# Performance work log

Hardware: AMD Instinct MI355X
Metric: run time of the kernel (lower is better)

Reference implementation:

```python
import jax, jax.numpy as jnp
import numpy as np

SCALE = 1.0 / (100.0 ** 0.5)  # module hard-codes QK / sqrt(100)


def setup_inputs() -> dict:
    key = jax.random.key(0)
    k1, k2, k3 = jax.random.split(key, 3)
    B, S, D = 8, 2048, 512
    head_size = 64
    x = jax.random.normal(k1, (B, S, D), dtype=jnp.float32)
    kernel = jax.random.normal(k2, (3, D, head_size), dtype=jnp.float32) * 0.02
    dense = jax.random.normal(k3, (D, D), dtype=jnp.float32) * 0.02
    return {"x": x, "kernel": kernel, "dense": dense, "heads": 8}


def reference(x, kernel, dense, heads):
    # All heads use the SAME kernel slices in the original loop, so each
    # iteration produces an identical V; compute once and tile.
    WQ = jnp.einsum('bsd,dh->bsh', x, kernel[0])  # [B,S,Hd]
    WK = jnp.einsum('bsd,dh->bsh', x, kernel[1])
    WV = jnp.einsum('bsd,dh->bsh', x, kernel[2])
    scores = jnp.einsum('bqh,bkh->bqk', WQ, WK) * SCALE  # [B,S,S]
    attn = jax.nn.softmax(scores, axis=-1)
    V = jnp.einsum('bqk,bkh->bqh', attn, WV)  # [B,S,Hd]
    out = jnp.tile(V, (1, 1, heads))  # concat of identical heads -> [B,S,heads*Hd]
    return jnp.einsum('bsf,fo->bso', out, dense)
```

## Files before the change

kernel.cpp:

```cpp
#include <hip/hip_runtime.h>
#include <math.h>


typedef __bf16 bf16;
typedef __bf16 bf16x4v __attribute__((ext_vector_type(4)));
typedef __bf16 bf16x8v __attribute__((ext_vector_type(8)));
typedef float f32x4 __attribute__((ext_vector_type(4)));

namespace {
constexpr int kS = 2048;
constexpr int kD = 512;
constexpr int kH = 64;
constexpr int kRows = 16384;
}

#define MFMA16(a, b, c) __builtin_amdgcn_mfma_f32_16x16x32_bf16((a), (b), (c), 0, 0, 0)

__global__ __launch_bounds__(256) void prep_kernel(const float* __restrict__ w,
                                                   const float* __restrict__ dense,
                                                   bf16* __restrict__ wtg,
                                                   float* __restrict__ dr) {
  int idx = blockIdx.x * 256 + threadIdx.x;
  if (idx < 98304) {
    int mat = idx >> 15, rem = idx & 32767;
    int n = rem >> 9, k = rem & 511;
    wtg[idx] = (bf16)w[mat * 32768 + k * 64 + n];
  } else {
    int e = idx - 98304;
    int j = e >> 9, o = e & 511;
    float s = 0.f;
#pragma unroll
    for (int h = 0; h < 8; ++h) s += dense[(size_t)(h * 64 + j) * kD + o];
    dr[e] = s;
  }
}

__global__ __launch_bounds__(256) void proj_kernel(const float* __restrict__ x,
                                                   const bf16* __restrict__ wtg,
                                                   bf16* __restrict__ wq,
                                                   bf16* __restrict__ wk,
                                                   bf16* __restrict__ wvt) {
  const int bt = blockIdx.x;
  const int tid = threadIdx.x;
  const int w = tid >> 6, tx = tid & 15, quad = (tid >> 4) & 3;
  const int row0 = bt * 64;

  __shared__ bf16 Xs[64 * 72];
  __shared__ bf16 Wts[3 * 64 * 72];

  f32x4 acc[3][4];
#pragma unroll
  for (int m = 0; m < 3; ++m)
#pragma unroll
    for (int nt = 0; nt < 4; ++nt) acc[m][nt] = (f32x4){0.f, 0.f, 0.f, 0.f};

  for (int k0 = 0; k0 < kD; k0 += 64) {
    __syncthreads();
#pragma unroll
    for (int p = 0; p < 4; ++p) {
      int i4 = tid + p * 256;
      int r = i4 >> 4, c4 = (i4 & 15) * 4;
      float4 f = *(const float4*)&x[(size_t)(row0 + r) * kD + k0 + c4];
      bf16x4v h = {(bf16)f.x, (bf16)f.y, (bf16)f.z, (bf16)f.w};
      *(bf16x4v*)&Xs[r * 72 + c4] = h;
    }
#pragma unroll
    for (int p = 0; p < 6; ++p) {
      int cc = tid + p * 256;
      int mat = cc >> 9, rem = cc & 511;
      int n = rem >> 3, c8 = (rem & 7) * 8;
      *(uint4*)&Wts[(mat * 64 + n) * 72 + c8] =
          *(const uint4*)&wtg[(size_t)mat * 32768 + (size_t)n * 512 + k0 + c8];
    }
    __syncthreads();
#pragma unroll
    for (int s = 0; s < 2; ++s) {
      bf16x8v a = *(bf16x8v*)&Xs[(w * 16 + tx) * 72 + s * 32 + quad * 8];
#pragma unroll
      for (int m = 0; m < 3; ++m)
#pragma unroll
        for (int nt = 0; nt < 4; ++nt) {
          bf16x8v bfr =
              *(bf16x8v*)&Wts[(m * 64 + nt * 16 + tx) * 72 + s * 32 + quad * 8];
          acc[m][nt] = MFMA16(a, bfr, acc[m][nt]);
        }
    }
  }

#pragma unroll
  for (int nt = 0; nt < 4; ++nt)
#pragma unroll
    for (int r = 0; r < 4; ++r) {
      int row_g = row0 + w * 16 + quad * 4 + r;
      int col = nt * 16 + tx;
      wq[(size_t)row_g * 64 + col] = (bf16)acc[0][nt][r];
      wk[(size_t)row_g * 64 + col] = (bf16)acc[1][nt][r];
    }
  __syncthreads();
  bf16* Vt = Xs;
#pragma unroll
  for (int nt = 0; nt < 4; ++nt)
#pragma unroll
    for (int r = 0; r < 4; ++r)
      Vt[(nt * 16 + tx) * 72 + (w * 16 + quad * 4 + r)] = (bf16)acc[2][nt][r];
  __syncthreads();
#pragma unroll
  for (int p = 0; p < 2; ++p) {
    int c = tid + p * 256;
    int v = c >> 3, seg = c & 7;
    *(uint4*)&wvt[(size_t)v * kRows + row0 + seg * 8] =
        *(uint4*)&Vt[v * 72 + seg * 8];
  }
}

__global__ __launch_bounds__(256, 4) void flash_kernel(
    const bf16* __restrict__ wq, const bf16* __restrict__ wk,
    const bf16* __restrict__ wvt, float* __restrict__ vo) {
  const int bid = blockIdx.x;
  const int b = bid & 7, qb = bid >> 3;
  const int q0 = qb * 16;
  const int tid = threadIdx.x;
  const int w = tid >> 6, lane = tid & 63, tx = tid & 15, quad = (tid >> 4) & 3;

  __shared__ __align__(16) char lds[38912];
  bf16* Qs = (bf16*)lds;
  bf16* Ksw = (bf16*)(lds + 2048 + w * 4096);
  bf16* Vtw = (bf16*)(lds + 18432 + w * 4096);
  bf16* Psw = (bf16*)(lds + 34816 + w * 1024);

  const bf16* wqb = wq + (size_t)(b * kS) * 64;
  const bf16* wkb = wk + (size_t)(b * kS) * 64;
  const bf16* wvb = wvt + b * kS;

  if (tid < 128) {
    int r = tid >> 3, lc = tid & 7;
    *(uint4*)&Qs[r * 64 + ((lc ^ (r & 7)) * 8)] =
        *(const uint4*)&wqb[(size_t)(q0 + r) * 64 + lc * 8];
  }
  __syncthreads();

  const int kc0 = (quad ^ (tx & 7)) * 8;
  const int kc1 = ((4 + quad) ^ (tx & 7)) * 8;
  const int h2 = (tx ^ (tx >> 2)) & 3;

  bf16x8v aq0 = *(bf16x8v*)&Qs[tx * 64 + kc0];
  bf16x8v aq1 = *(bf16x8v*)&Qs[tx * 64 + kc1];

  f32x4 oacc[4];
#pragma unroll
  for (int nt = 0; nt < 4; ++nt) oacc[nt] = (f32x4){0.f, 0.f, 0.f, 0.f};
  float lsum[4] = {0.f, 0.f, 0.f, 0.f};

  const int ksr = lane >> 3, kslc = lane & 7;
  const int vsv = lane >> 2, vsck = lane & 3;

  for (int t = 0; t < 16; ++t) {
    const int k0 = (t * 4 + w) * 32;
#pragma unroll
    for (int j = 0; j < 4; ++j) {
      int r = ksr + j * 8;
      *(uint4*)&Ksw[r * 64 + ((kslc ^ (r & 7)) * 8)] =
          *(const uint4*)&wkb[(size_t)(k0 + r) * 64 + kslc * 8];
      int v = vsv + j * 16;
      *(uint4*)&Vtw[v * 32 + ((vsck ^ ((v ^ (v >> 2)) & 3)) * 8)] =
          *(const uint4*)&wvb[(size_t)v * kRows + k0 + vsck * 8];
    }

#pragma unroll
    for (int nt = 0; nt < 2; ++nt) {
      int krow = nt * 16 + tx;
      bf16x8v b0 = *(bf16x8v*)&Ksw[krow * 64 + kc0];
      bf16x8v b1 = *(bf16x8v*)&Ksw[krow * 64 + kc1];
      f32x4 z = (f32x4){0.f, 0.f, 0.f, 0.f};
      z = MFMA16(aq0, b0, z);
      z = MFMA16(aq1, b1, z);
#pragma unroll
      for (int r = 0; r < 4; ++r) {
        float p = __expf(z[r] * 0.1f);
        lsum[r] += p;
        int q = quad * 4 + r;
        int chunk = nt * 2 + (tx >> 3);
        Psw[q * 32 + ((chunk ^ (r ^ quad)) * 8) + (tx & 7)] = (bf16)p;
      }
    }

    bf16x8v pa = *(bf16x8v*)&Psw[tx * 32 + ((quad ^ h2) * 8)];
#pragma unroll
    for (int nt = 0; nt < 4; ++nt) {
      bf16x8v vb = *(bf16x8v*)&Vtw[(nt * 16 + tx) * 32 + ((quad ^ h2) * 8)];
      oacc[nt] = MFMA16(pa, vb, oacc[nt]);
    }
  }

  __syncthreads();
  float* myO = (float*)(lds + 2048 + w * 4096);
  float* myL = (float*)(lds + 18432 + w * 64);
#pragma unroll
  for (int nt = 0; nt < 4; ++nt)
#pragma unroll
    for (int r = 0; r < 4; ++r)
      myO[(quad * 4 + r) * 64 + nt * 16 + tx] = oacc[nt][r];
#pragma unroll
  for (int r = 0; r < 4; ++r) {
    float v = lsum[r];
#pragma unroll
    for (int m = 1; m < 16; m <<= 1) v += __shfl_xor(v, m, 64);
    if (tx == 0) myL[quad * 4 + r] = v;
  }
  __syncthreads();

#pragma unroll
  for (int p = 0; p < 4; ++p) {
    int e = tid + p * 256;
    int row = e >> 6;
    float s = 0.f, lt = 0.f;
#pragma unroll
    for (int wv = 0; wv < 4; ++wv) {
      s += ((const float*)(lds + 2048 + wv * 4096))[e];
      lt += ((const float*)(lds + 18432 + wv * 64))[row];
    }
    vo[(size_t)(b * kS + q0 + row) * 64 + (e & 63)] = s / lt;
  }
}

__global__ __launch_bounds__(256) void out_gemm_kernel(
    const float* __restrict__ v, const float* __restrict__ dr,
    float* __restrict__ out) {
  const int rt = blockIdx.x, ct = blockIdx.y;
  const int tid = threadIdx.x;
  const int tx = tid & 15, ty = tid >> 4;

  __shared__ float As[64][68];
  __shared__ float Bs[64][68];

#pragma unroll
  for (int p = 0; p < 4; ++p) {
    int f4 = tid + p * 256;
    int r = f4 >> 4, c = (f4 & 15) * 4;
    *(float4*)&As[r][c] = *(const float4*)(v + (size_t)(rt * 64 + r) * kH + c);
    *(float4*)&Bs[r][c] = *(const float4*)(dr + (size_t)r * kD + ct * 64 + c);
  }
  __syncthreads();

  float acc[4][4] = {};
#pragma unroll
  for (int k = 0; k < 64; k += 4) {
    float a[4][4], bb[4][4];
#pragma unroll
    for (int i = 0; i < 4; ++i) {
      float4 t = *(const float4*)&As[ty * 4 + i][k];
      a[i][0] = t.x; a[i][1] = t.y; a[i][2] = t.z; a[i][3] = t.w;
    }
#pragma unroll
    for (int kk = 0; kk < 4; ++kk) {
      float4 t = *(const float4*)&Bs[k + kk][tx * 4];
      bb[kk][0] = t.x; bb[kk][1] = t.y; bb[kk][2] = t.z; bb[kk][3] = t.w;
    }
#pragma unroll
    for (int i = 0; i < 4; ++i)
#pragma unroll
      for (int kk = 0; kk < 4; ++kk)
#pragma unroll
        for (int j = 0; j < 4; ++j)
          acc[i][j] = fmaf(a[i][kk], bb[kk][j], acc[i][j]);
  }
#pragma unroll
  for (int i = 0; i < 4; ++i) {
    float4 vv = make_float4(acc[i][0], acc[i][1], acc[i][2], acc[i][3]);
    *(float4*)(out + (size_t)(rt * 64 + ty * 4 + i) * kD + ct * 64 + tx * 4) = vv;
  }
}

extern "C" void kernel_launch(void* const* d_in, const int* in_sizes, int n_in,
                              void* d_out, int out_size, void* d_ws,
                              size_t ws_size, hipStream_t stream) {
  const float* x = (const float*)d_in[0];
  const float* w = (const float*)d_in[1];
  const float* dense = (const float*)d_in[2];
  float* out = (float*)d_out;

  bf16* wq = (bf16*)d_ws;
  bf16* wk = wq + (size_t)kRows * 64;
  bf16* wvt = wk + (size_t)kRows * 64;
  bf16* wtg = wvt + (size_t)kRows * 64;
  float* dr = (float*)(wtg + 98304);
  float* vo = dr + 32768;

  prep_kernel<<<512, 256, 0, stream>>>(w, dense, wtg, dr);
  proj_kernel<<<256, 256, 0, stream>>>(x, wtg, wq, wk, wvt);
  flash_kernel<<<1024, 256, 0, stream>>>(wq, wk, wvt, vo);
  out_gemm_kernel<<<dim3(kRows / 64, kD / 64), 256, 0, stream>>>(vo, dr, out);
}
```

Measured before the change: 142.4 us.

## Process 32 query rows per flash block with 8 waves reusing K/V tiles

```diff
diff --git a/kernel.cpp b/kernel.cpp
--- a/kernel.cpp
+++ b/kernel.cpp
@@ -113,49 +113,49 @@
   }
 }
 
-__global__ __launch_bounds__(256, 4) void flash_kernel(
+__global__ __launch_bounds__(512, 4) void flash_kernel(
     const bf16* __restrict__ wq, const bf16* __restrict__ wk,
     const bf16* __restrict__ wvt, float* __restrict__ vo) {
   const int bid = blockIdx.x;
   const int b = bid & 7, qb = bid >> 3;
-  const int q0 = qb * 16;
+  const int q0 = qb * 32;
   const int tid = threadIdx.x;
   const int w = tid >> 6, lane = tid & 63, tx = tid & 15, quad = (tid >> 4) & 3;
 
-  __shared__ __align__(16) char lds[38912];
-  bf16* Qs = (bf16*)lds;
-  bf16* Ksw = (bf16*)(lds + 2048 + w * 4096);
-  bf16* Vtw = (bf16*)(lds + 18432 + w * 4096);
-  bf16* Psw = (bf16*)(lds + 34816 + w * 1024);
+  __shared__ __align__(16) char lds[65536];
+  __shared__ float Lsh[256];
+  bf16* Ksw = (bf16*)(lds + w * 8192);
+  bf16* Psw = Ksw;
+  bf16* Vtw = (bf16*)(lds + w * 8192 + 4096);
 
   const bf16* wqb = wq + (size_t)(b * kS) * 64;
   const bf16* wkb = wk + (size_t)(b * kS) * 64;
   const bf16* wvb = wvt + b * kS;
 
-  if (tid < 128) {
-    int r = tid >> 3, lc = tid & 7;
-    *(uint4*)&Qs[r * 64 + ((lc ^ (r & 7)) * 8)] =
-        *(const uint4*)&wqb[(size_t)(q0 + r) * 64 + lc * 8];
-  }
-  __syncthreads();
-
   const int kc0 = (quad ^ (tx & 7)) * 8;
   const int kc1 = ((4 + quad) ^ (tx & 7)) * 8;
   const int h2 = (tx ^ (tx >> 2)) & 3;
 
-  bf16x8v aq0 = *(bf16x8v*)&Qs[tx * 64 + kc0];
-  bf16x8v aq1 = *(bf16x8v*)&Qs[tx * 64 + kc1];
-
-  f32x4 oacc[4];
-#pragma unroll
-  for (int nt = 0; nt < 4; ++nt) oacc[nt] = (f32x4){0.f, 0.f, 0.f, 0.f};
-  float lsum[4] = {0.f, 0.f, 0.f, 0.f};
+  bf16x8v aq[2][2];
+#pragma unroll
+  for (int rt = 0; rt < 2; ++rt)
+#pragma unroll
+    for (int s = 0; s < 2; ++s)
+      aq[rt][s] = *(const bf16x8v*)&wqb[(size_t)(q0 + rt * 16 + tx) * 64 +
+                                        s * 32 + quad * 8];
+
+  f32x4 oacc[2][4];
+#pragma unroll
+  for (int rt = 0; rt < 2; ++rt)
+#pragma unroll
+    for (int nt = 0; nt < 4; ++nt) oacc[rt][nt] = (f32x4){0.f, 0.f, 0.f, 0.f};
+  float lsum[2][4] = {};
 
   const int ksr = lane >> 3, kslc = lane & 7;
   const int vsv = lane >> 2, vsck = lane & 3;
 
-  for (int t = 0; t < 16; ++t) {
-    const int k0 = (t * 4 + w) * 32;
+  for (int t = 0; t < 8; ++t) {
+    const int k0 = (t * 8 + w) * 32;
 #pragma unroll
     for (int j = 0; j < 4; ++j) {
       int r = ksr + j * 8;
@@ -171,53 +171,63 @@
       int krow = nt * 16 + tx;
       bf16x8v b0 = *(bf16x8v*)&Ksw[krow * 64 + kc0];
       bf16x8v b1 = *(bf16x8v*)&Ksw[krow * 64 + kc1];
-      f32x4 z = (f32x4){0.f, 0.f, 0.f, 0.f};
-      z = MFMA16(aq0, b0, z);
-      z = MFMA16(aq1, b1, z);
-#pragma unroll
-      for (int r = 0; r < 4; ++r) {
-        float p = __expf(z[r] * 0.1f);
-        lsum[r] += p;
-        int q = quad * 4 + r;
-        int chunk = nt * 2 + (tx >> 3);
-        Psw[q * 32 + ((chunk ^ (r ^ quad)) * 8) + (tx & 7)] = (bf16)p;
+#pragma unroll
+      for (int rt = 0; rt < 2; ++rt) {
+        f32x4 z = (f32x4){0.f, 0.f, 0.f, 0.f};
+        z = MFMA16(aq[rt][0], b0, z);
+        z = MFMA16(aq[rt][1], b1, z);
+#pragma unroll
+        for (int r = 0; r < 4; ++r) {
+          float p = __expf(z[r] * 0.1f);
+          lsum[rt][r] += p;
+          int q = rt * 16 + quad * 4 + r;
+          int chunk = nt * 2 + (tx >> 3);
+          Psw[q * 32 + ((chunk ^ (r ^ quad)) * 8) + (tx & 7)] = (bf16)p;
+        }
       }
     }
 
-    bf16x8v pa = *(bf16x8v*)&Psw[tx * 32 + ((quad ^ h2) * 8)];
-#pragma unroll
-    for (int nt = 0; nt < 4; ++nt) {
-      bf16x8v vb = *(bf16x8v*)&Vtw[(nt * 16 + tx) * 32 + ((quad ^ h2) * 8)];
-      oacc[nt] = MFMA16(pa, vb, oacc[nt]);
-    }
-  }
-
-  __syncthreads();
-  float* myO = (float*)(lds + 2048 + w * 4096);
-  float* myL = (float*)(lds + 18432 + w * 64);
-#pragma unroll
-  for (int nt = 0; nt < 4; ++nt)
-#pragma unroll
-    for (int r = 0; r < 4; ++r)
-      myO[(quad * 4 + r) * 64 + nt * 16 + tx] = oacc[nt][r];
-#pragma unroll
-  for (int r = 0; r < 4; ++r) {
-    float v = lsum[r];
-#pragma unroll
-    for (int m = 1; m < 16; m <<= 1) v += __shfl_xor(v, m, 64);
-    if (tx == 0) myL[quad * 4 + r] = v;
-  }
+#pragma unroll
+    for (int rt = 0; rt < 2; ++rt) {
+      bf16x8v pa = *(bf16x8v*)&Psw[(rt * 16 + tx) * 32 + ((quad ^ h2) * 8)];
+#pragma unroll
+      for (int nt = 0; nt < 4; ++nt) {
+        bf16x8v vb = *(bf16x8v*)&Vtw[(nt * 16 + tx) * 32 + ((quad ^ h2) * 8)];
+        oacc[rt][nt] = MFMA16(pa, vb, oacc[rt][nt]);
+      }
+    }
+  }
+
+  __syncthreads();
+  float* myO = (float*)(lds + w * 8192);
+  float* myL = Lsh + w * 32;
+#pragma unroll
+  for (int rt = 0; rt < 2; ++rt)
+#pragma unroll
+    for (int nt = 0; nt < 4; ++nt)
+#pragma unroll
+      for (int r = 0; r < 4; ++r)
+        myO[(rt * 16 + quad * 4 + r) * 64 + nt * 16 + tx] = oacc[rt][nt][r];
+#pragma unroll
+  for (int rt = 0; rt < 2; ++rt)
+#pragma unroll
+    for (int r = 0; r < 4; ++r) {
+      float v = lsum[rt][r];
+#pragma unroll
+      for (int m = 1; m < 16; m <<= 1) v += __shfl_xor(v, m, 64);
+      if (tx == 0) myL[rt * 16 + quad * 4 + r] = v;
+    }
   __syncthreads();
 
 #pragma unroll
   for (int p = 0; p < 4; ++p) {
-    int e = tid + p * 256;
+    int e = tid + p * 512;
     int row = e >> 6;
     float s = 0.f, lt = 0.f;
 #pragma unroll
-    for (int wv = 0; wv < 4; ++wv) {
-      s += ((const float*)(lds + 2048 + wv * 4096))[e];
-      lt += ((const float*)(lds + 18432 + wv * 64))[row];
+    for (int wv = 0; wv < 8; ++wv) {
+      s += ((const float*)(lds + wv * 8192))[e];
+      lt += Lsh[wv * 32 + row];
     }
     vo[(size_t)(b * kS + q0 + row) * 64 + (e & 63)] = s / lt;
   }
@@ -288,6 +298,6 @@
 
   prep_kernel<<<512, 256, 0, stream>>>(w, dense, wtg, dr);
   proj_kernel<<<256, 256, 0, stream>>>(x, wtg, wq, wk, wvt);
-  flash_kernel<<<1024, 256, 0, stream>>>(wq, wk, wvt, vo);
+  flash_kernel<<<512, 512, 0, stream>>>(wq, wk, wvt, vo);
   out_gemm_kernel<<<dim3(kRows / 64, kD / 64), 256, 0, stream>>>(vo, dr, out);
 }
```

New measurement: 142.5 us. About the same (+0.1%).
